# Kernel optimization log

Hardware: AMD Instinct MI355X
Metric: run time of the kernel (lower is better)

## Reference

```python
import jax, jax.numpy as jnp
import numpy as np

N_NODES = 24
BATCH = 65536

def _build_edge_index():
    # hard-coded 24-node supply-chain DAG from the source: node i (i<22, even pair)
    # connects to nodes 2*(i//2)+2 and 2*(i//2)+3
    rows, cols = [], []
    for i in range(22):
        base = 2 * (i // 2) + 2
        rows += [i, i]
        cols += [base, base + 1]
    return jnp.asarray(np.stack([rows, cols]), dtype=jnp.int64)  # [2, 44]


def setup_inputs() -> dict:
    key = jax.random.key(0)
    ks = jax.random.split(key, 4)
    x = jax.random.normal(ks[0], (BATCH, N_NODES, 10), dtype=jnp.float32)
    W1 = jax.random.normal(ks[1], (10, 64), dtype=jnp.float32) * (1.0 / np.sqrt(10))
    b1 = jnp.zeros((64,), dtype=jnp.float32)
    W3 = jax.random.normal(ks[2], (64, 64), dtype=jnp.float32) * (1.0 / 8.0)
    b3 = jnp.zeros((64,), dtype=jnp.float32)
    W2 = jax.random.normal(ks[3], (64, 10), dtype=jnp.float32) * (1.0 / 8.0)
    b2 = jnp.zeros((10,), dtype=jnp.float32)
    edge_index = _build_edge_index()
    return {"x": x, "W1": W1, "b1": b1, "W3": W3, "b3": b3,
            "W2": W2, "b2": b2, "edge_index": edge_index}


def _gcn_norm(edge_index, n_nodes):
    # PyG gcn_norm with add_self_loops=True: deg counted at target (col) index
    src, dst = edge_index[0], edge_index[1]
    deg = jnp.ones((n_nodes,), jnp.float32).at[dst].add(1.0)  # self loop contributes 1
    dinv = jax.lax.rsqrt(deg)
    norm_e = dinv[src] * dinv[dst]        # [E] edge weights
    norm_self = dinv * dinv               # [N] self-loop weights
    return src, dst, norm_e, norm_self


def _gcn_conv(h, W, b, src, dst, norm_e, norm_self):
    # h: [B, N, Fin] -> [B, N, Fout]
    hw = h @ W                                             # [B, N, Fout]
    msg = hw[:, src, :] * norm_e[None, :, None]            # gather + scale [B, E, Fout]
    agg = jnp.zeros_like(hw).at[:, dst, :].add(msg)        # scatter-add over targets
    agg = agg + hw * norm_self[None, :, None]              # self loops
    return agg + b


def reference(x, W1, b1, W3, b3, W2, b2, edge_index):
    src, dst, norm_e, norm_self = _gcn_norm(edge_index, x.shape[1])
    h = jax.nn.relu(_gcn_conv(x, W1, b1, src, dst, norm_e, norm_self))
    h = jax.nn.relu(_gcn_conv(h, W3, b3, src, dst, norm_e, norm_self))
    msg = jax.nn.relu(_gcn_conv(h, W2, b2, src, dst, norm_e, norm_self))  # [B, N, 10]
    pool = jnp.mean(msg, axis=1)  # global_mean_pool over the 24 nodes -> [B, 10]
    return pool
```

## Files before the change

### kernel.cpp

```cpp
#include <hip/hip_runtime.h>
#include <hip/hip_bf16.h>


typedef __attribute__((ext_vector_type(8))) short bf16x8;
typedef __attribute__((ext_vector_type(4))) float f32x4;

#define NBLK  1024
#define ITERS 8

__device__ __forceinline__ unsigned short f2bf(float f) {
  __hip_bfloat16 h = __float2bfloat16(f);
  return __builtin_bit_cast(unsigned short, h);
}

union U16 { uint4 u; bf16x8 b; };

__device__ __forceinline__ bf16x8 pack8(const float v[8]) {
  U16 un;
  un.u.x = (unsigned)f2bf(v[0]) | ((unsigned)f2bf(v[1]) << 16);
  un.u.y = (unsigned)f2bf(v[2]) | ((unsigned)f2bf(v[3]) << 16);
  un.u.z = (unsigned)f2bf(v[4]) | ((unsigned)f2bf(v[5]) << 16);
  un.u.w = (unsigned)f2bf(v[6]) | ((unsigned)f2bf(v[7]) << 16);
  return un.b;
}
__device__ __forceinline__ uint2 pk4(f32x4 a) {
  uint2 r;
  r.x = (unsigned)f2bf(a[0]) | ((unsigned)f2bf(a[1]) << 16);
  r.y = (unsigned)f2bf(a[2]) | ((unsigned)f2bf(a[3]) << 16);
  return r;
}
__device__ __forceinline__ uint2 pk4r(f32x4 a) {
  const f32x4 z = {0.f, 0.f, 0.f, 0.f};
  return pk4(__builtin_elementwise_max(a, z));
}

__global__ __launch_bounds__(256, 2)
void gnn_kernel(const float* __restrict__ xg,  const float* __restrict__ w1g,
                const float* __restrict__ b1g, const float* __restrict__ w3g,
                const float* __restrict__ b3g, const float* __restrict__ w2g,
                const float* __restrict__ b2g, float* __restrict__ outg) {
  __shared__ __align__(16) unsigned short bufA_s[4][64 * 72];
  __shared__ __align__(16) unsigned short bufB_s[4][48 * 72];
  __shared__ __align__(16) unsigned short bufD_s[4][16 * 72];

  const int tid  = threadIdx.x;
  const int w    = tid >> 6;
  const int lane = tid & 63;
  const int l15  = lane & 15;
  const int g    = lane >> 4;
  unsigned short* bA = bufA_s[w];
  unsigned short* bB = bufB_s[w];
  unsigned short* bD = bufD_s[w];
  const int wgid = blockIdx.x * 4 + w;

  bf16x8 w1bf[4], w3f[4][2], w2f[2], amixB[3][2];
  {
    float v[8];
    #pragma unroll
    for (int nc = 0; nc < 4; ++nc) {
      #pragma unroll
      for (int j = 0; j < 8; ++j) { int k = 8 * g + j; v[j] = (k < 10) ? w1g[k * 64 + 16 * nc + l15] : 0.f; }
      w1bf[nc] = pack8(v);
      #pragma unroll
      for (int ks = 0; ks < 2; ++ks) {
        #pragma unroll
        for (int j = 0; j < 8; ++j) v[j] = w3g[(32 * ks + 8 * g + j) * 64 + 16 * nc + l15] * (1.f / 3.f);
        w3f[nc][ks] = pack8(v);
      }
    }
    #pragma unroll
    for (int ks = 0; ks < 2; ++ks) {
      #pragma unroll
      for (int j = 0; j < 8; ++j) {
        int k = 32 * ks + 8 * g + j;
        v[j] = (l15 < 10) ? w2g[k * 10 + l15] * (1.f / 3.f) : 0.f;
      }
      w2f[ks] = pack8(v);
    }
    #pragma unroll
    for (int nn = 0; nn < 3; ++nn) {
      #pragma unroll
      for (int ks = 0; ks < 2; ++ks) {
        #pragma unroll
        for (int j = 0; j < 8; ++j) {
          const int k = 32 * ks + 8 * g + j, n = 16 * nn + l15;
          float c = 0.f;
          if (k == 48) c = 3.f;
          else if (k < 48 && (k / 24) == (n / 24)) {
            const int s = k % 24, t = n % 24;
            if (t < 2)      c = (s == t) ? 3.f : 0.f;
            else if (t < 4) c = (s == t) ? 1.f : ((s < 2) ? 1.7320508075688772f : 0.f);
            else { const int sa = (t & ~1) - 2; c = (s == t || s == sa || s == sa + 1) ? 1.f : 0.f; }
          }
          v[j] = c;
        }
        amixB[nn][ks] = pack8(v);
      }
    }
  }

  const unsigned short b1f = f2bf(b1g[lane]);
  const unsigned short b3f = f2bf(b3g[lane]);

  {
    const uint4 z4 = {0, 0, 0, 0};
    *(uint4*)&bA[lane * 72 + 48] = z4;
    *(uint4*)&bA[lane * 72 + 56] = z4;
    *(uint4*)&bA[lane * 72 + 64] = z4;
    if (lane < 16) {
      *(uint4*)&bD[lane * 72 + 48] = z4;
      *(uint4*)&bD[lane * 72 + 56] = z4;
      *(uint4*)&bD[lane * 72 + 64] = z4;
      bD[lane * 72 + 48] = (lane < 10) ? f2bf(b2g[lane]) : (unsigned short)0;
    }
  }

  int xoff[3];
  #pragma unroll
  for (int mt = 0; mt < 3; ++mt) {
    const int r = 16 * mt + l15, sub = r / 24, n = r - 24 * sub;
    xoff[mt] = sub * 240 + n * 10;
  }

  const f32x4 zf = {0.f, 0.f, 0.f, 0.f};

  for (int it = 0; it < ITERS; ++it) {
    const int sp = wgid * 16 + it * 2;
    const float* xb = xg + (long)sp * 240;

    bA[lane * 72 + 48] = b1f;

    f32x4 acc1[3][4];
    #pragma unroll
    for (int mt = 0; mt < 3; ++mt) {
      float v[8] = {0.f, 0.f, 0.f, 0.f, 0.f, 0.f, 0.f, 0.f};
      const float* xr = xb + xoff[mt];
      if (g == 0) {
        float2 p0 = *(const float2*)(xr + 0);
        float2 p1 = *(const float2*)(xr + 2);
        float2 p2 = *(const float2*)(xr + 4);
        float2 p3 = *(const float2*)(xr + 6);
        v[0] = p0.x; v[1] = p0.y; v[2] = p1.x; v[3] = p1.y;
        v[4] = p2.x; v[5] = p2.y; v[6] = p3.x; v[7] = p3.y;
      } else if (g == 1) {
        float2 p4 = *(const float2*)(xr + 8);
        v[0] = p4.x; v[1] = p4.y;
      }
      bf16x8 ax = pack8(v);
      #pragma unroll
      for (int nc = 0; nc < 4; ++nc)
        acc1[mt][nc] = __builtin_amdgcn_mfma_f32_16x16x32_bf16(ax, w1bf[nc], zf, 0, 0, 0);
    }
    #pragma unroll
    for (int mt = 0; mt < 3; ++mt)
      #pragma unroll
      for (int nc = 0; nc < 4; ++nc)
        *(uint2*)&bA[(16 * nc + l15) * 72 + 16 * mt + 4 * g] = pk4(acc1[mt][nc]);

    U16 a2[4][2];
    #pragma unroll
    for (int mi = 0; mi < 4; ++mi)
      #pragma unroll
      for (int ks = 0; ks < 2; ++ks)
        a2[mi][ks].u = *(const uint4*)&bA[(16 * mi + l15) * 72 + 32 * ks + 8 * g];
    bA[lane * 72 + 48] = b3f;
    f32x4 acc2[4][3];
    #pragma unroll
    for (int mi = 0; mi < 4; ++mi)
      #pragma unroll
      for (int nn = 0; nn < 3; ++nn) {
        f32x4 t = __builtin_amdgcn_mfma_f32_16x16x32_bf16(a2[mi][0].b, amixB[nn][0], zf, 0, 0, 0);
        acc2[mi][nn] = __builtin_amdgcn_mfma_f32_16x16x32_bf16(a2[mi][1].b, amixB[nn][1], t, 0, 0, 0);
      }
    #pragma unroll
    for (int mi = 0; mi < 4; ++mi)
      #pragma unroll
      for (int nn = 0; nn < 3; ++nn)
        *(uint2*)&bB[(16 * nn + l15) * 72 + 16 * mi + 4 * g] = pk4r(acc2[mi][nn]);

    U16 a3[3][2];
    #pragma unroll
    for (int mt = 0; mt < 3; ++mt)
      #pragma unroll
      for (int ks = 0; ks < 2; ++ks)
        a3[mt][ks].u = *(const uint4*)&bB[(16 * mt + l15) * 72 + 32 * ks + 8 * g];
    f32x4 acc3[3][4];
    #pragma unroll
    for (int mt = 0; mt < 3; ++mt)
      #pragma unroll
      for (int nc = 0; nc < 4; ++nc) {
        f32x4 t = __builtin_amdgcn_mfma_f32_16x16x32_bf16(a3[mt][0].b, w3f[nc][0], zf, 0, 0, 0);
        acc3[mt][nc] = __builtin_amdgcn_mfma_f32_16x16x32_bf16(a3[mt][1].b, w3f[nc][1], t, 0, 0, 0);
      }
    #pragma unroll
    for (int mt = 0; mt < 3; ++mt)
      #pragma unroll
      for (int nc = 0; nc < 4; ++nc)
        *(uint2*)&bA[(16 * nc + l15) * 72 + 16 * mt + 4 * g] = pk4(acc3[mt][nc]);

    U16 a4[4][2];
    #pragma unroll
    for (int mi = 0; mi < 4; ++mi)
      #pragma unroll
      for (int ks = 0; ks < 2; ++ks)
        a4[mi][ks].u = *(const uint4*)&bA[(16 * mi + l15) * 72 + 32 * ks + 8 * g];
    f32x4 acc4[4][3];
    #pragma unroll
    for (int mi = 0; mi < 4; ++mi)
      #pragma unroll
      for (int nn = 0; nn < 3; ++nn) {
        f32x4 t = __builtin_amdgcn_mfma_f32_16x16x32_bf16(a4[mi][0].b, amixB[nn][0], zf, 0, 0, 0);
        acc4[mi][nn] = __builtin_amdgcn_mfma_f32_16x16x32_bf16(a4[mi][1].b, amixB[nn][1], t, 0, 0, 0);
      }
    #pragma unroll
    for (int mi = 0; mi < 4; ++mi)
      #pragma unroll
      for (int nn = 0; nn < 3; ++nn)
        *(uint2*)&bB[(16 * nn + l15) * 72 + 16 * mi + 4 * g] = pk4r(acc4[mi][nn]);

    U16 a5[3][2];
    #pragma unroll
    for (int mt = 0; mt < 3; ++mt)
      #pragma unroll
      for (int ks = 0; ks < 2; ++ks)
        a5[mt][ks].u = *(const uint4*)&bB[(16 * mt + l15) * 72 + 32 * ks + 8 * g];
    f32x4 acc5[3];
    #pragma unroll
    for (int mt = 0; mt < 3; ++mt) {
      f32x4 t = __builtin_amdgcn_mfma_f32_16x16x32_bf16(a5[mt][0].b, w2f[0], zf, 0, 0, 0);
      acc5[mt] = __builtin_amdgcn_mfma_f32_16x16x32_bf16(a5[mt][1].b, w2f[1], t, 0, 0, 0);
    }
    #pragma unroll
    for (int mt = 0; mt < 3; ++mt)
      *(uint2*)&bD[l15 * 72 + 16 * mt + 4 * g] = pk4(acc5[mt]);

    U16 a6[2];
    #pragma unroll
    for (int ks = 0; ks < 2; ++ks)
      a6[ks].u = *(const uint4*)&bD[l15 * 72 + 32 * ks + 8 * g];
    f32x4 acc6[3];
    #pragma unroll
    for (int nt = 0; nt < 3; ++nt) {
      f32x4 t = __builtin_amdgcn_mfma_f32_16x16x32_bf16(a6[0].b, amixB[nt][0], zf, 0, 0, 0);
      acc6[nt] = __builtin_amdgcn_mfma_f32_16x16x32_bf16(a6[1].b, amixB[nt][1], t, 0, 0, 0);
    }

    {
      f32x4 v0 = __builtin_elementwise_max(acc6[0], zf);
      f32x4 v1 = __builtin_elementwise_max(acc6[1], zf);
      f32x4 v2 = __builtin_elementwise_max(acc6[2], zf);
      f32x4 sum0 = v0, sum1 = v2;
      if (l15 < 8) sum0 += v1; else sum1 += v1;
      #pragma unroll
      for (int d = 1; d < 16; d <<= 1) {
        #pragma unroll
        for (int r = 0; r < 4; ++r) {
          sum0[r] += __shfl_xor(sum0[r], d);
          sum1[r] += __shfl_xor(sum1[r], d);
        }
      }
      if (l15 < 2) {
        const f32x4 s = (l15 == 0) ? sum0 : sum1;
        const float sc = 1.f / 72.f;
        const long  so = (long)(sp + l15) * 10;
        if (g < 3) { float2 t0 = {s[0] * sc, s[1] * sc}; *(float2*)&outg[so + 4 * g] = t0; }
        if (g < 2) { float2 t1 = {s[2] * sc, s[3] * sc}; *(float2*)&outg[so + 4 * g + 2] = t1; }
      }
    }
  }
}

extern "C" void kernel_launch(void* const* d_in, const int* in_sizes, int n_in,
                              void* d_out, int out_size, void* d_ws, size_t ws_size,
                              hipStream_t stream) {
  (void)in_sizes; (void)n_in; (void)d_ws; (void)ws_size; (void)out_size;
  const float* x  = (const float*)d_in[0];
  const float* W1 = (const float*)d_in[1];
  const float* b1 = (const float*)d_in[2];
  const float* W3 = (const float*)d_in[3];
  const float* b3 = (const float*)d_in[4];
  const float* W2 = (const float*)d_in[5];
  const float* b2 = (const float*)d_in[6];
  float* out = (float*)d_out;
  hipLaunchKernelGGL(gnn_kernel, dim3(NBLK), dim3(256), 0, stream,
                     x, W1, b1, W3, b3, W2, b2, out);
}
```

Measured before the change: 183.5 us.

## Prefetch next iteration's x tile into registers and use cheaper bf16 packing

Loads the x features for iteration it+1 into registers while the current iteration computes, so global-load latency overlaps the MFMA and LDS work. It also replaces the per-element float-to-bf16 conversion with a round-half-up add plus a byte permute that packs two values in one instruction. The prefetch raises register pressure, which could hurt occupancy under launch_bounds(256,2). The new rounding skips round-to-nearest-even and NaN handling, so results can differ slightly in the last bf16 bit.

```diff
diff --git a/kernel.cpp b/kernel.cpp
--- a/kernel.cpp
+++ b/kernel.cpp
@@ -12,21 +12,26 @@
   __hip_bfloat16 h = __float2bfloat16(f);
   return __builtin_bit_cast(unsigned short, h);
 }
+__device__ __forceinline__ unsigned bpack(float lo, float hi) {
+  unsigned ulo = __builtin_bit_cast(unsigned, lo) + 0x8000u;
+  unsigned uhi = __builtin_bit_cast(unsigned, hi) + 0x8000u;
+  return __builtin_amdgcn_perm(uhi, ulo, 0x07060302u);
+}
 
 union U16 { uint4 u; bf16x8 b; };
 
 __device__ __forceinline__ bf16x8 pack8(const float v[8]) {
   U16 un;
-  un.u.x = (unsigned)f2bf(v[0]) | ((unsigned)f2bf(v[1]) << 16);
-  un.u.y = (unsigned)f2bf(v[2]) | ((unsigned)f2bf(v[3]) << 16);
-  un.u.z = (unsigned)f2bf(v[4]) | ((unsigned)f2bf(v[5]) << 16);
-  un.u.w = (unsigned)f2bf(v[6]) | ((unsigned)f2bf(v[7]) << 16);
+  un.u.x = bpack(v[0], v[1]);
+  un.u.y = bpack(v[2], v[3]);
+  un.u.z = bpack(v[4], v[5]);
+  un.u.w = bpack(v[6], v[7]);
   return un.b;
 }
 __device__ __forceinline__ uint2 pk4(f32x4 a) {
   uint2 r;
-  r.x = (unsigned)f2bf(a[0]) | ((unsigned)f2bf(a[1]) << 16);
-  r.y = (unsigned)f2bf(a[2]) | ((unsigned)f2bf(a[3]) << 16);
+  r.x = bpack(a[0], a[1]);
+  r.y = bpack(a[2], a[3]);
   return r;
 }
 __device__ __forceinline__ uint2 pk4r(f32x4 a) {
@@ -122,35 +127,50 @@
     xoff[mt] = sub * 240 + n * 10;
   }
 
+  float2 px[3][4];
+  auto loadX = [&](const float* xb) {
+    #pragma unroll
+    for (int mt = 0; mt < 3; ++mt) {
+      const float* xr = xb + xoff[mt];
+      if (g == 0) {
+        px[mt][0] = *(const float2*)(xr + 0);
+        px[mt][1] = *(const float2*)(xr + 2);
+        px[mt][2] = *(const float2*)(xr + 4);
+        px[mt][3] = *(const float2*)(xr + 6);
+      } else if (g == 1) {
+        px[mt][0] = *(const float2*)(xr + 8);
+      }
+    }
+  };
+  loadX(xg + (long)(wgid * 16) * 240);
+
   const f32x4 zf = {0.f, 0.f, 0.f, 0.f};
 
   for (int it = 0; it < ITERS; ++it) {
     const int sp = wgid * 16 + it * 2;
-    const float* xb = xg + (long)sp * 240;
 
     bA[lane * 72 + 48] = b1f;
 
-    f32x4 acc1[3][4];
+    bf16x8 ax[3];
     #pragma unroll
     for (int mt = 0; mt < 3; ++mt) {
       float v[8] = {0.f, 0.f, 0.f, 0.f, 0.f, 0.f, 0.f, 0.f};
-      const float* xr = xb + xoff[mt];
       if (g == 0) {
-        float2 p0 = *(const float2*)(xr + 0);
-        float2 p1 = *(const float2*)(xr + 2);
-        float2 p2 = *(const float2*)(xr + 4);
-        float2 p3 = *(const float2*)(xr + 6);
-        v[0] = p0.x; v[1] = p0.y; v[2] = p1.x; v[3] = p1.y;
-        v[4] = p2.x; v[5] = p2.y; v[6] = p3.x; v[7] = p3.y;
+        v[0] = px[mt][0].x; v[1] = px[mt][0].y; v[2] = px[mt][1].x; v[3] = px[mt][1].y;
+        v[4] = px[mt][2].x; v[5] = px[mt][2].y; v[6] = px[mt][3].x; v[7] = px[mt][3].y;
       } else if (g == 1) {
-        float2 p4 = *(const float2*)(xr + 8);
-        v[0] = p4.x; v[1] = p4.y;
-      }
-      bf16x8 ax = pack8(v);
+        v[0] = px[mt][0].x; v[1] = px[mt][0].y;
+      }
+      ax[mt] = pack8(v);
+    }
+    if (it + 1 < ITERS) loadX(xg + (long)(sp + 2) * 240);
+
+    f32x4 acc1[3][4];
+    #pragma unroll
+    for (int mt = 0; mt < 3; ++mt)
       #pragma unroll
       for (int nc = 0; nc < 4; ++nc)
-        acc1[mt][nc] = __builtin_amdgcn_mfma_f32_16x16x32_bf16(ax, w1bf[nc], zf, 0, 0, 0);
-    }
+        acc1[mt][nc] = __builtin_amdgcn_mfma_f32_16x16x32_bf16(ax[mt], w1bf[nc], zf, 0, 0, 0);
     #pragma unroll
     for (int mt = 0; mt < 3; ++mt)
       #pragma unroll
```

Result: slower. 205.3 us (+11.9%).
